# Performance work log

Hardware: AMD Instinct MI355X
Metric: run time of the kernel (lower is better)

## Reference

```python
import jax, jax.numpy as jnp
import numpy as np

T = 0.1      # temperature
P = 3        # no_of_pos_eles
K = 3        # no_of_neg_eles
NC = 4       # number of semantic classes in synthetic labels
LAM = 0.1    # lamda_local
EPS = 1e-8


def setup_inputs():
    key = jax.random.key(0)
    k1, k2 = jax.random.split(key)
    B, C, H, W = 8, 256, 128, 128
    features = jax.random.normal(k1, (B, C, H, W), dtype=jnp.float32)
    labels = jax.random.randint(k2, (B, H, W), 0, NC, dtype=jnp.int32)
    return {"features": features, "labels": labels}


def _forward(features, labels):
    B, C, H, W = features.shape
    N = H * W
    # per-pixel L2 normalize over channels (F.normalize dim=1, eps=1e-12)
    f = features / jnp.maximum(jnp.linalg.norm(features, axis=1, keepdims=True), 1e-12)
    f = f.reshape(B, C, N).transpose(0, 2, 1)                    # (B, N, C), unit rows
    lab = labels.reshape(B, N)
    cls_mask = lab[:, None, :] == jnp.arange(NC)[None, :, None]  # (B, NC, N)
    counts = cls_mask.sum(-1)                                    # (B, NC)

    keys = jax.random.split(jax.random.key(42), 5)

    def sample(k, n):
        # uniform random subset of n pixels of each class via top-k of iid uniforms
        u = jax.random.uniform(k, (B, NC, N))
        idx = jax.lax.top_k(jnp.where(cls_mask, u, -jnp.inf), n)[1]       # (B, NC, n)
        return jnp.take_along_axis(f[:, None], idx[..., None], axis=2)    # (B, NC, n, C)

    off = ~jnp.eye(NC, dtype=bool)                                        # neg_cls != cls
    neg_valid = jnp.arange(K)[None, None, :] < jnp.minimum(counts, K)[..., None]  # (B,NC,K)
    nmask = neg_valid[:, None, None] & off[None, :, None, :, None]        # (B,NC,1,NC,K)
    has_neg = ((counts > 0)[:, None, :] & off[None]).any(-1)              # (B, NC)

    def neg_sum(anchors, negs):
        # anchors (B,NC,P,C) unit rows, negs (B,NC,K,C) unit rows -> (B,NC,P)
        d = jnp.einsum('bcpd,bekd->bcpek', anchors, negs) / T
        return jnp.sum(jnp.exp(d) * nmask, axis=(-1, -2))

    def unit(v):
        return v / jnp.maximum(jnp.linalg.norm(v, axis=-1, keepdims=True), EPS)

    # ---- part 1: within-image contrast ----
    pos = sample(keys[0], P)                                     # (B,NC,P,C)
    neg = sample(keys[1], K)                                     # (B,NC,K,C)
    mu1 = unit(pos.mean(2))                                      # (B,NC,C)
    sp1 = jnp.exp(jnp.einsum('bcpd,bcd->bcp', pos, mu1) / T)     # (B,NC,P)
    sn1 = neg_sum(pos, neg)                                      # (B,NC,P)
    valid1 = ((counts >= P) & has_neg)[..., None]                # (B,NC,1)
    loss = jnp.sum(-jnp.log(sp1 / (sp1 + sn1 + EPS)) * valid1)

    # ---- part 2: cross-image contrast (local_loss_exp_no == 1, B >= 2) ----
    pos1 = sample(keys[2], P)                                    # anchors from b1
    mu2 = unit(sample(keys[3], P).mean(2))                       # (B,NC,C), means from b2
    neg1 = sample(keys[4], K)                                    # negatives from b1
    sp2 = jnp.exp(jnp.einsum('bcpd,acd->bacp', pos1, mu2) / T)   # (b1,b2,NC,P)
    sn2 = neg_sum(pos1, neg1)                                    # (b1,NC,P)
    enough = counts >= P
    valid2 = (enough[:, None, :] & enough[None, :, :] & has_neg[:, None, :]
              & (~jnp.eye(B, dtype=bool))[..., None])            # (b1,b2,NC)
    loss += jnp.sum(-jnp.log(sp2 / (sp2 + sn2[:, None] + EPS)) * valid2[..., None])

    return LAM * loss / (B * P + EPS)


def reference(features, labels):
    return _forward(features, labels)
```

## Files before the change

### kernel.cpp

```cpp
#include <hip/hip_runtime.h>
#include <stdint.h>


namespace {

constexpr int Nn = 16384;

__device__ __forceinline__ uint32_t rotl32(uint32_t v, int d) {
  return (v << d) | (v >> (32 - d));
}

__device__ __forceinline__ void threefry2x32(uint32_t k0, uint32_t k1,
                                             uint32_t x0, uint32_t x1,
                                             uint32_t& o0, uint32_t& o1) {
  uint32_t ks2 = k0 ^ k1 ^ 0x1BD11BDAu;
  x0 += k0; x1 += k1;
#define TF_R(d) { x0 += x1; x1 = rotl32(x1, (d)); x1 ^= x0; }
  TF_R(13) TF_R(15) TF_R(26) TF_R(6)
  x0 += k1; x1 += ks2 + 1u;
  TF_R(17) TF_R(29) TF_R(16) TF_R(24)
  x0 += ks2; x1 += k0 + 2u;
  TF_R(13) TF_R(15) TF_R(26) TF_R(6)
  x0 += k0; x1 += k1 + 3u;
  TF_R(17) TF_R(29) TF_R(16) TF_R(24)
  x0 += k1; x1 += ks2 + 4u;
  TF_R(13) TF_R(15) TF_R(26) TF_R(6)
  x0 += ks2; x1 += k0 + 5u;
#undef TF_R
  o0 = x0; o1 = x1;
}

__device__ __forceinline__ void ins3(unsigned long long t[3], unsigned long long k) {
  if (k > t[0])      { t[2] = t[1]; t[1] = t[0]; t[0] = k; }
  else if (k > t[1]) { t[2] = t[1]; t[1] = k; }
  else if (k > t[2]) { t[2] = k; }
}

__global__ void topk_kernel(const int4* __restrict__ labels4,
                            int* __restrict__ idx_buf,
                            int* __restrict__ counts) {
  const int g = blockIdx.x;
  const int s = g >> 5;
  const int b = (g >> 2) & 7;
  const int c = g & 3;

  uint32_t sk0, sk1;
  threefry2x32(0u, 42u, 0u, (uint32_t)s, sk0, sk1);

  unsigned long long t[3] = {0ull, 0ull, 0ull};
  int cnt = 0;
  const int4* row = labels4 + b * (Nn / 4);
  const uint32_t jbase = (uint32_t)((b * 4 + c) * Nn);
#pragma unroll 4
  for (int it = 0; it < 16; ++it) {
    const int i4 = threadIdx.x + it * 256;
    const int4 L = row[i4];
    const int la[4] = {L.x, L.y, L.z, L.w};
#pragma unroll
    for (int e = 0; e < 4; ++e) {
      const uint32_t n = (uint32_t)(i4 * 4 + e);
      uint32_t r0, r1;
      threefry2x32(sk0, sk1, 0u, jbase + n, r0, r1);
      const uint32_t bits = r0 ^ r1;
      const uint32_t fb = (bits >> 9) | 0x3f800000u;
      const bool m = (la[e] == c);
      const unsigned long long key =
          m ? (((unsigned long long)fb << 32) |
               (unsigned long long)(0xFFFFFFFFu - n))
            : 0ull;
      cnt += m ? 1 : 0;
      ins3(t, key);
    }
  }

  for (int off = 32; off > 0; off >>= 1) {
    unsigned long long o0 = __shfl_down(t[0], (unsigned)off);
    unsigned long long o1 = __shfl_down(t[1], (unsigned)off);
    unsigned long long o2 = __shfl_down(t[2], (unsigned)off);
    int oc = __shfl_down(cnt, (unsigned)off);
    ins3(t, o0); ins3(t, o1); ins3(t, o2);
    cnt += oc;
  }
  __shared__ unsigned long long sm[4][3];
  __shared__ int sc[4];
  const int lane = threadIdx.x & 63;
  const int wave = threadIdx.x >> 6;
  if (lane == 0) { sm[wave][0] = t[0]; sm[wave][1] = t[1]; sm[wave][2] = t[2]; sc[wave] = cnt; }
  __syncthreads();
  if (threadIdx.x == 0) {
    unsigned long long f[3] = {sm[0][0], sm[0][1], sm[0][2]};
    int tot = sc[0];
    for (int w = 1; w < 4; ++w) {
      ins3(f, sm[w][0]); ins3(f, sm[w][1]); ins3(f, sm[w][2]);
      tot += sc[w];
    }
#pragma unroll
    for (int r = 0; r < 3; ++r) {
      const int n = (f[r] == 0ull) ? 0
                    : (int)(0xFFFFFFFFu - (uint32_t)(f[r] & 0xFFFFFFFFull));
      idx_buf[g * 3 + r] = n;
    }
    if (s == 0) counts[b * 4 + c] = tot;
  }
}

__global__ void gather_mu_kernel(const float* __restrict__ feat,
                                 const int* __restrict__ idx_buf,
                                 float* __restrict__ fnorm,
                                 float* __restrict__ mu) {
  const int g = blockIdx.x;
  const int ch = threadIdx.x;
  const int lane = threadIdx.x & 63, wave = threadIdx.x >> 6;
  __shared__ float sr[4][4];
  __shared__ float sr2[4];

  if (g < 480) {
    const int b = (g / 12) & 7;
    const int n = idx_buf[g];
    const float v = feat[((b << 8) + ch) * Nn + n];
    float ss = v * v;
    for (int off = 32; off > 0; off >>= 1) ss += __shfl_down(ss, (unsigned)off);
    if (lane == 0) sr[wave][0] = ss;
    __syncthreads();
    const float nrm = fmaxf(sqrtf(sr[0][0] + sr[1][0] + sr[2][0] + sr[3][0]), 1e-12f);
    fnorm[g * 256 + ch] = v / nrm;
  } else {
    const int gm = g - 480;
    const int m = gm >> 5;
    const int bc = gm & 31;
    const int b = bc >> 2;
    const int s = m ? 3 : 0;
    const int ib = (s * 32 + bc) * 3;
    float v[3], ss[3];
#pragma unroll
    for (int r = 0; r < 3; ++r) {
      const int n = idx_buf[ib + r];
      v[r] = feat[((b << 8) + ch) * Nn + n];
      ss[r] = v[r] * v[r];
    }
    for (int off = 32; off > 0; off >>= 1) {
#pragma unroll
      for (int r = 0; r < 3; ++r) ss[r] += __shfl_down(ss[r], (unsigned)off);
    }
    if (lane == 0) {
#pragma unroll
      for (int r = 0; r < 3; ++r) sr[wave][r] = ss[r];
    }
    __syncthreads();
    float f = 0.f;
#pragma unroll
    for (int r = 0; r < 3; ++r) {
      const float nrm = fmaxf(sqrtf(sr[0][r] + sr[1][r] + sr[2][r] + sr[3][r]), 1e-12f);
      f += v[r] / nrm;
    }
    f /= 3.0f;
    float s2 = f * f;
    for (int off = 32; off > 0; off >>= 1) s2 += __shfl_down(s2, (unsigned)off);
    if (lane == 0) sr2[wave] = s2;
    __syncthreads();
    const float nrm2 = fmaxf(sqrtf(sr2[0] + sr2[1] + sr2[2] + sr2[3]), 1e-8f);
    mu[gm * 256 + ch] = f / nrm2;
  }
}

__global__ void loss_kernel(const float* __restrict__ fnorm,
                            const float* __restrict__ mu,
                            const int* __restrict__ counts,
                            float* __restrict__ partials) {
  const int g = blockIdx.x;
  const int b = g / 12;
  const int c = (g % 12) / 3;
  const int p = g % 3;
  const int ch = threadIdx.x;
  const int bc = b * 4 + c;

  const float a1 = fnorm[(bc * 3 + p) * 256 + ch];
  const float a2 = fnorm[((64 + bc) * 3 + p) * 256 + ch];

  float part[33];
  part[0] = a1 * mu[bc * 256 + ch];
#pragma unroll
  for (int e = 0; e < 4; ++e)
#pragma unroll
    for (int k = 0; k < 3; ++k)
      part[1 + e * 3 + k] = a1 * fnorm[((32 + b * 4 + e) * 3 + k) * 256 + ch];
#pragma unroll
  for (int b2 = 0; b2 < 8; ++b2)
    part[13 + b2] = a2 * mu[(32 + b2 * 4 + c) * 256 + ch];
#pragma unroll
  for (int e = 0; e < 4; ++e)
#pragma unroll
    for (int k = 0; k < 3; ++k)
      part[21 + e * 3 + k] = a2 * fnorm[((128 + b * 4 + e) * 3 + k) * 256 + ch];

  for (int off = 32; off > 0; off >>= 1) {
#pragma unroll
    for (int i = 0; i < 33; ++i) part[i] += __shfl_down(part[i], (unsigned)off);
  }
  __shared__ float red[4][33];
  const int lane = threadIdx.x & 63, wave = threadIdx.x >> 6;
  if (lane == 0) {
#pragma unroll
    for (int i = 0; i < 33; ++i) red[wave][i] = part[i];
  }
  __syncthreads();

  if (threadIdx.x == 0) {
    float d[33];
#pragma unroll
    for (int i = 0; i < 33; ++i) d[i] = red[0][i] + red[1][i] + red[2][i] + red[3][i];

    int cb[4];
    for (int e = 0; e < 4; ++e) cb[e] = counts[b * 4 + e];
    bool has_neg = false;
    for (int e = 0; e < 4; ++e) if (e != c && cb[e] > 0) has_neg = true;
    const bool valid_anchor = (cb[c] >= 3) && has_neg;

    float sn1 = 0.f, sn2 = 0.f;
    for (int e = 0; e < 4; ++e) {
      if (e == c) continue;
      int km = cb[e] < 3 ? cb[e] : 3;
      for (int k = 0; k < km; ++k) {
        sn1 += expf(d[1 + e * 3 + k] * 10.0f);
        sn2 += expf(d[21 + e * 3 + k] * 10.0f);
      }
    }
    float term = 0.f;
    if (valid_anchor) {
      float sp1 = expf(d[0] * 10.0f);
      term -= logf(sp1 / (sp1 + sn1 + 1e-8f));
      for (int b2 = 0; b2 < 8; ++b2) {
        if (b2 == b) continue;
        if (counts[b2 * 4 + c] >= 3) {
          float sp2 = expf(d[13 + b2] * 10.0f);
          term -= logf(sp2 / (sp2 + sn2 + 1e-8f));
        }
      }
    }
    partials[g] = term;
  }
}

__global__ void finalize_kernel(const float* __restrict__ partials,
                                float* __restrict__ out) {
  const int t = threadIdx.x;
  float v = (t < 96) ? partials[t] : 0.f;
  for (int off = 32; off > 0; off >>= 1) v += __shfl_down(v, (unsigned)off);
  __shared__ float s2[2];
  if ((t & 63) == 0) s2[t >> 6] = v;
  __syncthreads();
  if (t == 0) {
    double total = (double)s2[0] + (double)s2[1];
    out[0] = (float)(0.1 * total / (24.0 + 1e-8));
  }
}

}

extern "C" void kernel_launch(void* const* d_in, const int* in_sizes, int n_in,
                              void* d_out, int out_size, void* d_ws, size_t ws_size,
                              hipStream_t stream) {
  const float* feat = (const float*)d_in[0];
  const int* labels = (const int*)d_in[1];
  float* out = (float*)d_out;
  char* ws = (char*)d_ws;

  int* idx_buf    = (int*)(ws);
  int* counts     = (int*)(ws + 1920);
  float* fnorm    = (float*)(ws + 2048);
  float* mu       = (float*)(ws + 493568);
  float* partials = (float*)(ws + 559104);

  topk_kernel<<<160, 256, 0, stream>>>((const int4*)labels, idx_buf, counts);
  gather_mu_kernel<<<544, 256, 0, stream>>>(feat, idx_buf, fnorm, mu);
  loss_kernel<<<96, 256, 0, stream>>>(fnorm, mu, counts, partials);
  finalize_kernel<<<1, 128, 0, stream>>>(partials, out);
}
```

Baseline: 201.1 us.

## Fuse top-k sampling with feature gather and fold finalize into loss via atomics

Merges the top-k selection kernel with the feature gather/normalize kernel, so each block gathers and normalizes its own three sampled pixels, and widens blocks to 512 threads. The separate mu computation is dropped: the loss kernel recomputes the class means from the normalized samples and applies their norm algebraically. The finalize kernel is replaced by an atomic accumulate with a last-block ticket. This cuts the launch count from four to two and removes intermediate buffers. In exchange it adds atomic ordering concerns and float atomic summation order nondeterminism, and it relies on block 0 resetting the accumulator before any loss block runs.

```diff
diff --git a/kernel.cpp b/kernel.cpp
--- a/kernel.cpp
+++ b/kernel.cpp
@@ -36,13 +36,18 @@
   else if (k > t[2]) { t[2] = k; }
 }
 
-__global__ void topk_kernel(const int4* __restrict__ labels4,
-                            int* __restrict__ idx_buf,
-                            int* __restrict__ counts) {
+__global__ void topk_gather_kernel(const int4* __restrict__ labels4,
+                                   const float* __restrict__ feat,
+                                   int* __restrict__ counts,
+                                   float* __restrict__ fnorm,
+                                   float* __restrict__ acc,
+                                   int* __restrict__ ticket) {
   const int g = blockIdx.x;
   const int s = g >> 5;
   const int b = (g >> 2) & 7;
   const int c = g & 3;
+
+  if (g == 0 && threadIdx.x == 0) { acc[0] = 0.f; ticket[0] = 0; }
 
   uint32_t sk0, sk1;
   threefry2x32(0u, 42u, 0u, (uint32_t)s, sk0, sk1);
@@ -52,8 +57,8 @@
   const int4* row = labels4 + b * (Nn / 4);
   const uint32_t jbase = (uint32_t)((b * 4 + c) * Nn);
 #pragma unroll 4
-  for (int it = 0; it < 16; ++it) {
-    const int i4 = threadIdx.x + it * 256;
+  for (int it = 0; it < 8; ++it) {
+    const int i4 = threadIdx.x + it * 512;
     const int4 L = row[i4];
     const int la[4] = {L.x, L.y, L.z, L.w};
 #pragma unroll
@@ -81,8 +86,10 @@
     ins3(t, o0); ins3(t, o1); ins3(t, o2);
     cnt += oc;
   }
-  __shared__ unsigned long long sm[4][3];
-  __shared__ int sc[4];
+  __shared__ unsigned long long sm[8][3];
+  __shared__ int sc[8];
+  __shared__ int sidx[3];
+  __shared__ float sr[4][3];
   const int lane = threadIdx.x & 63;
   const int wave = threadIdx.x >> 6;
   if (lane == 0) { sm[wave][0] = t[0]; sm[wave][1] = t[1]; sm[wave][2] = t[2]; sc[wave] = cnt; }
@@ -90,52 +97,26 @@
   if (threadIdx.x == 0) {
     unsigned long long f[3] = {sm[0][0], sm[0][1], sm[0][2]};
     int tot = sc[0];
-    for (int w = 1; w < 4; ++w) {
+    for (int w = 1; w < 8; ++w) {
       ins3(f, sm[w][0]); ins3(f, sm[w][1]); ins3(f, sm[w][2]);
       tot += sc[w];
     }
 #pragma unroll
     for (int r = 0; r < 3; ++r) {
-      const int n = (f[r] == 0ull) ? 0
-                    : (int)(0xFFFFFFFFu - (uint32_t)(f[r] & 0xFFFFFFFFull));
-      idx_buf[g * 3 + r] = n;
+      sidx[r] = (f[r] == 0ull) ? 0
+                : (int)(0xFFFFFFFFu - (uint32_t)(f[r] & 0xFFFFFFFFull));
     }
     if (s == 0) counts[b * 4 + c] = tot;
   }
-}
-
-__global__ void gather_mu_kernel(const float* __restrict__ feat,
-                                 const int* __restrict__ idx_buf,
-                                 float* __restrict__ fnorm,
-                                 float* __restrict__ mu) {
-  const int g = blockIdx.x;
-  const int ch = threadIdx.x;
-  const int lane = threadIdx.x & 63, wave = threadIdx.x >> 6;
-  __shared__ float sr[4][4];
-  __shared__ float sr2[4];
-
-  if (g < 480) {
-    const int b = (g / 12) & 7;
-    const int n = idx_buf[g];
-    const float v = feat[((b << 8) + ch) * Nn + n];
-    float ss = v * v;
-    for (int off = 32; off > 0; off >>= 1) ss += __shfl_down(ss, (unsigned)off);
-    if (lane == 0) sr[wave][0] = ss;
-    __syncthreads();
-    const float nrm = fmaxf(sqrtf(sr[0][0] + sr[1][0] + sr[2][0] + sr[3][0]), 1e-12f);
-    fnorm[g * 256 + ch] = v / nrm;
-  } else {
-    const int gm = g - 480;
-    const int m = gm >> 5;
-    const int bc = gm & 31;
-    const int b = bc >> 2;
-    const int s = m ? 3 : 0;
-    const int ib = (s * 32 + bc) * 3;
-    float v[3], ss[3];
+  __syncthreads();
+
+  float v[3];
+  if (threadIdx.x < 256) {
+    const int ch = threadIdx.x;
+    float ss[3];
 #pragma unroll
     for (int r = 0; r < 3; ++r) {
-      const int n = idx_buf[ib + r];
-      v[r] = feat[((b << 8) + ch) * Nn + n];
+      v[r] = feat[((b << 8) + ch) * Nn + sidx[r]];
       ss[r] = v[r] * v[r];
     }
     for (int off = 32; off > 0; off >>= 1) {
@@ -146,27 +127,23 @@
 #pragma unroll
       for (int r = 0; r < 3; ++r) sr[wave][r] = ss[r];
     }
-    __syncthreads();
-    float f = 0.f;
+  }
+  __syncthreads();
+  if (threadIdx.x < 256) {
+    const int ch = threadIdx.x;
 #pragma unroll
     for (int r = 0; r < 3; ++r) {
       const float nrm = fmaxf(sqrtf(sr[0][r] + sr[1][r] + sr[2][r] + sr[3][r]), 1e-12f);
-      f += v[r] / nrm;
-    }
-    f /= 3.0f;
-    float s2 = f * f;
-    for (int off = 32; off > 0; off >>= 1) s2 += __shfl_down(s2, (unsigned)off);
-    if (lane == 0) sr2[wave] = s2;
-    __syncthreads();
-    const float nrm2 = fmaxf(sqrtf(sr2[0] + sr2[1] + sr2[2] + sr2[3]), 1e-8f);
-    mu[gm * 256 + ch] = f / nrm2;
+      fnorm[(g * 3 + r) * 256 + ch] = v[r] / nrm;
+    }
   }
 }
 
 __global__ void loss_kernel(const float* __restrict__ fnorm,
-                            const float* __restrict__ mu,
                             const int* __restrict__ counts,
-                            float* __restrict__ partials) {
+                            float* __restrict__ acc,
+                            int* __restrict__ ticket,
+                            float* __restrict__ out) {
   const int g = blockIdx.x;
   const int b = g / 12;
   const int c = (g % 12) / 3;
@@ -177,38 +154,49 @@
   const float a1 = fnorm[(bc * 3 + p) * 256 + ch];
   const float a2 = fnorm[((64 + bc) * 3 + p) * 256 + ch];
 
-  float part[33];
-  part[0] = a1 * mu[bc * 256 + ch];
+  const float f1 = fnorm[(bc * 3 + 0) * 256 + ch] +
+                   fnorm[(bc * 3 + 1) * 256 + ch] +
+                   fnorm[(bc * 3 + 2) * 256 + ch];
+
+  float part[42];
+  part[0] = a1 * f1;
+  part[1] = f1 * f1;
 #pragma unroll
   for (int e = 0; e < 4; ++e)
 #pragma unroll
     for (int k = 0; k < 3; ++k)
-      part[1 + e * 3 + k] = a1 * fnorm[((32 + b * 4 + e) * 3 + k) * 256 + ch];
-#pragma unroll
-  for (int b2 = 0; b2 < 8; ++b2)
-    part[13 + b2] = a2 * mu[(32 + b2 * 4 + c) * 256 + ch];
+      part[2 + e * 3 + k] = a1 * fnorm[((32 + b * 4 + e) * 3 + k) * 256 + ch];
+#pragma unroll
+  for (int b2 = 0; b2 < 8; ++b2) {
+    const int ib = (96 + b2 * 4 + c) * 3;
+    const float f2 = fnorm[(ib + 0) * 256 + ch] +
+                     fnorm[(ib + 1) * 256 + ch] +
+                     fnorm[(ib + 2) * 256 + ch];
+    part[14 + 2 * b2]     = a2 * f2;
+    part[14 + 2 * b2 + 1] = f2 * f2;
+  }
 #pragma unroll
   for (int e = 0; e < 4; ++e)
 #pragma unroll
     for (int k = 0; k < 3; ++k)
-      part[21 + e * 3 + k] = a2 * fnorm[((128 + b * 4 + e) * 3 + k) * 256 + ch];
+      part[30 + e * 3 + k] = a2 * fnorm[((128 + b * 4 + e) * 3 + k) * 256 + ch];
 
   for (int off = 32; off > 0; off >>= 1) {
 #pragma unroll
-    for (int i = 0; i < 33; ++i) part[i] += __shfl_down(part[i], (unsigned)off);
-  }
-  __shared__ float red[4][33];
+    for (int i = 0; i < 42; ++i) part[i] += __shfl_down(part[i], (unsigned)off);
+  }
+  __shared__ float red[4][42];
   const int lane = threadIdx.x & 63, wave = threadIdx.x >> 6;
   if (lane == 0) {
 #pragma unroll
-    for (int i = 0; i < 33; ++i) red[wave][i] = part[i];
+    for (int i = 0; i < 42; ++i) red[wave][i] = part[i];
   }
   __syncthreads();
 
   if (threadIdx.x == 0) {
-    float d[33];
-#pragma unroll
-    for (int i = 0; i < 33; ++i) d[i] = red[0][i] + red[1][i] + red[2][i] + red[3][i];
+    float d[42];
+#pragma unroll
+    for (int i = 0; i < 42; ++i) d[i] = red[0][i] + red[1][i] + red[2][i] + red[3][i];
 
     int cb[4];
     for (int e = 0; e < 4; ++e) cb[e] = counts[b * 4 + e];
@@ -221,37 +209,32 @@
       if (e == c) continue;
       int km = cb[e] < 3 ? cb[e] : 3;
       for (int k = 0; k < km; ++k) {
-        sn1 += expf(d[1 + e * 3 + k] * 10.0f);
-        sn2 += expf(d[21 + e * 3 + k] * 10.0f);
+        sn1 += expf(d[2 + e * 3 + k] * 10.0f);
+        sn2 += expf(d[30 + e * 3 + k] * 10.0f);
       }
     }
     float term = 0.f;
     if (valid_anchor) {
-      float sp1 = expf(d[0] * 10.0f);
+      const float d0 = (d[0] / 3.0f) / fmaxf(sqrtf(d[1]) / 3.0f, 1e-8f);
+      const float sp1 = expf(d0 * 10.0f);
       term -= logf(sp1 / (sp1 + sn1 + 1e-8f));
       for (int b2 = 0; b2 < 8; ++b2) {
         if (b2 == b) continue;
         if (counts[b2 * 4 + c] >= 3) {
-          float sp2 = expf(d[13 + b2] * 10.0f);
+          const float d2 = (d[14 + 2 * b2] / 3.0f) /
+                           fmaxf(sqrtf(d[14 + 2 * b2 + 1]) / 3.0f, 1e-8f);
+          const float sp2 = expf(d2 * 10.0f);
           term -= logf(sp2 / (sp2 + sn2 + 1e-8f));
         }
       }
     }
-    partials[g] = term;
-  }
-}
-
-__global__ void finalize_kernel(const float* __restrict__ partials,
-                                float* __restrict__ out) {
-  const int t = threadIdx.x;
-  float v = (t < 96) ? partials[t] : 0.f;
-  for (int off = 32; off > 0; off >>= 1) v += __shfl_down(v, (unsigned)off);
-  __shared__ float s2[2];
-  if ((t & 63) == 0) s2[t >> 6] = v;
-  __syncthreads();
-  if (t == 0) {
-    double total = (double)s2[0] + (double)s2[1];
-    out[0] = (float)(0.1 * total / (24.0 + 1e-8));
+    atomicAdd(acc, term);
+    __threadfence();
+    const int old = atomicAdd(ticket, 1);
+    if (old == 95) {
+      const float total = atomicAdd(acc, 0.0f);
+      out[0] = (float)(0.1 * (double)total / (24.0 + 1e-8));
+    }
   }
 }
 
@@ -265,14 +248,12 @@
   float* out = (float*)d_out;
   char* ws = (char*)d_ws;
 
-  int* idx_buf    = (int*)(ws);
-  int* counts     = (int*)(ws + 1920);
-  float* fnorm    = (float*)(ws + 2048);
-  float* mu       = (float*)(ws + 493568);
-  float* partials = (float*)(ws + 559104);
-
-  topk_kernel<<<160, 256, 0, stream>>>((const int4*)labels, idx_buf, counts);
-  gather_mu_kernel<<<544, 256, 0, stream>>>(feat, idx_buf, fnorm, mu);
-  loss_kernel<<<96, 256, 0, stream>>>(fnorm, mu, counts, partials);
-  finalize_kernel<<<1, 128, 0, stream>>>(partials, out);
-}
+  int* counts  = (int*)(ws);
+  float* fnorm = (float*)(ws + 1024);
+  float* acc   = (float*)(ws + 492544);
+  int* ticket  = (int*)(ws + 492548);
+
+  topk_gather_kernel<<<160, 512, 0, stream>>>((const int4*)labels, feat,
+                                              counts, fnorm, acc, ticket);
+  loss_kernel<<<96, 256, 0, stream>>>(fnorm, counts, acc, ticket, out);
+}
```

Result: faster. 196.4 us (median of 2 runs) (-2.4%).
